# Kernel tuning notes

Hardware: AMD Instinct MI355X
Metric: run time of the kernel (lower is better)

Reference implementation:

```python
import jax, jax.numpy as jnp
import numpy as np

EPS = 1e-6

def _rms(x, g):
    # RMSNorm over last dim (head_dim)
    return x * jax.lax.rsqrt(jnp.mean(x * x, axis=-1, keepdims=True) + EPS) * g

def _split_heads(x, h):
    b, l, hd = x.shape
    return x.reshape(b, l, h, hd // h).transpose(0, 2, 1, 3)  # b h l d

def setup_inputs() -> dict:
    key = jax.random.key(0)
    ks = jax.random.split(key, 10)
    B, Limg, Lip, D, Dip, Temb = 1, 2048, 512, 3072, 1280, 1280
    return {
        "ip_hidden_states": jax.random.normal(ks[0], (B, Lip, Dip), jnp.float32),
        "img_query": jax.random.normal(ks[1], (B, Limg, D), jnp.float32),
        "img_key": jax.random.normal(ks[2], (B, Limg, D), jnp.float32),
        "img_value": jax.random.normal(ks[3], (B, Limg, D), jnp.float32),
        "t_emb": jax.random.normal(ks[4], (B, Temb), jnp.float32),
        "w_ada": jax.random.normal(ks[5], (2 * Dip, Temb), jnp.float32) * 0.02,
        "b_ada": jnp.zeros((2 * Dip,), jnp.float32),
        "w_k_ip": jax.random.normal(ks[6], (D, Dip), jnp.float32) * 0.02,
        "w_v_ip": jax.random.normal(ks[7], (D, Dip), jnp.float32) * 0.02,
        "g_q": jnp.ones((128,), jnp.float32),
        "g_k": jnp.ones((128,), jnp.float32),
        "g_ipk": jnp.ones((128,), jnp.float32),
        "n_heads": 24,
    }

def reference(ip_hidden_states, img_query, img_key, img_value, t_emb,
              w_ada, b_ada, w_k_ip, w_v_ip, g_q, g_k, g_ipk, n_heads):
    # AdaLayerNorm ('normal' mode): silu + linear -> shift/scale, LayerNorm (no affine)
    e = jax.nn.silu(t_emb) @ w_ada.T + b_ada              # [B, 2*Dip]
    shift, scale = jnp.split(e, 2, axis=1)
    mu = jnp.mean(ip_hidden_states, axis=-1, keepdims=True)
    var = jnp.var(ip_hidden_states, axis=-1, keepdims=True)
    xn = (ip_hidden_states - mu) * jax.lax.rsqrt(var + EPS)
    ip_norm = xn * (1.0 + scale[:, None]) + shift[:, None]  # [B, Lip, Dip]

    ip_key = ip_norm @ w_k_ip.T                            # [B, Lip, D]
    ip_value = ip_norm @ w_v_ip.T

    q = _split_heads(img_query, n_heads)                   # [B, H, Limg, d]
    k = _split_heads(img_key, n_heads)
    v = _split_heads(img_value, n_heads)
    ipk = _split_heads(ip_key, n_heads)                    # [B, H, Lip, d]
    ipv = _split_heads(ip_value, n_heads)

    q = _rms(q, g_q)
    k = _rms(k, g_k)
    ipk = _rms(ipk, g_ipk)

    key_all = jnp.concatenate([k, ipk], axis=2)            # [B, H, Limg+Lip, d]
    val_all = jnp.concatenate([v, ipv], axis=2)

    d = q.shape[-1]
    scores = jnp.einsum('bhqd,bhkd->bhqk', q, key_all) * (1.0 / np.sqrt(d))
    probs = jax.nn.softmax(scores, axis=-1)
    out = jnp.einsum('bhqk,bhkd->bhqd', probs, val_all)    # [B, H, Limg, d]

    b, h, l, dd = out.shape
    return out.transpose(0, 2, 1, 3).reshape(b, l, h * dd)
```

## Files before the change

kernel.cpp:

```cpp
#include <hip/hip_runtime.h>
#include <math.h>

#define H    24
#define Dh   128
#define LIMG 2048
#define LIP  512
#define DM   3072
#define DIP  1280
#define LK   2560
#define EPSF 1e-6f
#define SM_SCALE 0.08838834764831845f
#define C2EXP 0.12751930f
#define THRU 90.50967f

#define EXP2F(x) __builtin_exp2f(x)

typedef __attribute__((ext_vector_type(8))) short bf16x8;
typedef __attribute__((ext_vector_type(4))) float f32x4;

typedef const unsigned int __attribute__((address_space(1))) gu32;
typedef unsigned int __attribute__((address_space(3))) lu32;

static __device__ __forceinline__ unsigned short f2bf(float x) {
  union { float f; unsigned u; } v; v.f = x;
  unsigned r = v.u + 0x7fffu + ((v.u >> 16) & 1u);
  return (unsigned short)(r >> 16);
}

static __device__ __forceinline__ float bf2f(unsigned short b) {
  union { unsigned u; float f; } v; v.u = ((unsigned)b) << 16;
  return v.f;
}

static __device__ __forceinline__ unsigned cvt_pk_bf16(float a, float b) {
  unsigned r;
  asm("v_cvt_pk_bf16_f32 %0, %1, %2" : "=v"(r) : "v"(a), "v"(b));
  return r;
}

__global__ __launch_bounds__(256) void ada_kernel(
    const float* __restrict__ t_emb, const float* __restrict__ w_ada,
    const float* __restrict__ b_ada, float* __restrict__ e) {
  int j = blockIdx.x;
  int tid = threadIdx.x;
  const float* wrow = w_ada + (long)j * DIP;
  float acc = 0.f;
  for (int k = tid; k < DIP; k += 256) {
    float t = t_emb[k];
    acc += (t / (1.f + expf(-t))) * wrow[k];
  }
#pragma unroll
  for (int m = 1; m < 64; m <<= 1) acc += __shfl_xor(acc, m, 64);
  __shared__ float red[4];
  if ((tid & 63) == 0) red[tid >> 6] = acc;
  __syncthreads();
  if (tid == 0) e[j] = red[0] + red[1] + red[2] + red[3] + b_ada[j];
}

__global__ __launch_bounds__(256) void adaln_kernel(
    const float* __restrict__ x, const float* __restrict__ e,
    unsigned short* __restrict__ ipnh, unsigned short* __restrict__ ipnl) {
  int r = blockIdx.x;
  int tid = threadIdx.x;
  const float* xr = x + (long)r * DIP;
  float v[5];
  float s = 0.f, ss = 0.f;
#pragma unroll
  for (int i = 0; i < 5; i++) {
    v[i] = xr[tid + i * 256];
    s += v[i];
    ss += v[i] * v[i];
  }
#pragma unroll
  for (int m = 1; m < 64; m <<= 1) {
    s += __shfl_xor(s, m, 64);
    ss += __shfl_xor(ss, m, 64);
  }
  __shared__ float rs_[4], rss_[4];
  if ((tid & 63) == 0) { rs_[tid >> 6] = s; rss_[tid >> 6] = ss; }
  __syncthreads();
  s = rs_[0] + rs_[1] + rs_[2] + rs_[3];
  ss = rss_[0] + rss_[1] + rss_[2] + rss_[3];
  float mu = s * (1.f / DIP);
  float var = ss * (1.f / DIP) - mu * mu;
  float rstd = rsqrtf(var + EPSF);
  unsigned short* oh = ipnh + (long)r * DIP;
  unsigned short* ol = ipnl + (long)r * DIP;
#pragma unroll
  for (int i = 0; i < 5; i++) {
    int c = tid + i * 256;
    float o = (v[i] - mu) * rstd * (1.f + e[DIP + c]) + e[c];
    unsigned short hb = f2bf(o);
    oh[c] = hb;
    ol[c] = f2bf(o - bf2f(hb));
  }
}

__global__ __launch_bounds__(256) void prep_kernel(
    const float* __restrict__ k_in, const float* __restrict__ v_in,
    const float* __restrict__ g_k,
    unsigned short* __restrict__ Kb, unsigned short* __restrict__ Vt) {
  __shared__ unsigned short Vls[128][33];
  int h = blockIdx.y, l0 = blockIdx.x * 32;
  int tid = threadIdx.x;
  int r = tid >> 3, c = tid & 7;
  const float* ksrc = k_in + (long)(l0 + r) * DM + h * Dh + c * 16;
  const float* vsrc = v_in + (long)(l0 + r) * DM + h * Dh + c * 16;
  float kv[16], vv[16];
  float ssq = 0.f;
#pragma unroll
  for (int i = 0; i < 4; i++) {
    float4 a = *(const float4*)(ksrc + i * 4);
    float4 b = *(const float4*)(vsrc + i * 4);
    kv[i*4+0]=a.x; kv[i*4+1]=a.y; kv[i*4+2]=a.z; kv[i*4+3]=a.w;
    vv[i*4+0]=b.x; vv[i*4+1]=b.y; vv[i*4+2]=b.z; vv[i*4+3]=b.w;
    ssq += a.x*a.x + a.y*a.y + a.z*a.z + a.w*a.w;
  }
  ssq += __shfl_xor(ssq, 1, 8);
  ssq += __shfl_xor(ssq, 2, 8);
  ssq += __shfl_xor(ssq, 4, 8);
  float rstd = rsqrtf(ssq * (1.f / Dh) + EPSF);
  unsigned short kb[16];
#pragma unroll
  for (int i = 0; i < 16; i++) kb[i] = f2bf(kv[i] * rstd * g_k[c * 16 + i]);
  unsigned short* kdst = Kb + ((long)h * LK + l0 + r) * Dh + c * 16;
  *(uint4*)(kdst) = *(uint4*)(kb);
  *(uint4*)(kdst + 8) = *(uint4*)(kb + 8);
#pragma unroll
  for (int i = 0; i < 16; i++) Vls[c * 16 + i][r] = f2bf(vv[i]);
  __syncthreads();
  if (tid < 128) {
    int d = tid;
    unsigned short ov[32];
#pragma unroll
    for (int j = 0; j < 32; j++) ov[j] = Vls[d][j];
    unsigned short* vdst = Vt + ((long)h * 80 + (l0 >> 5)) * 4096 + d * 32;
    *(uint4*)(vdst)      = *(uint4*)(ov);
    *(uint4*)(vdst + 8)  = *(uint4*)(ov + 8);
    *(uint4*)(vdst + 16) = *(uint4*)(ov + 16);
    *(uint4*)(vdst + 24) = *(uint4*)(ov + 24);
  }
}

__global__ __launch_bounds__(256) void proj_kernel(
    const unsigned short* __restrict__ Ah, const unsigned short* __restrict__ Al,
    const float* __restrict__ Wk, const float* __restrict__ Wv,
    const float* __restrict__ g_ipk,
    unsigned short* __restrict__ Kb, unsigned short* __restrict__ Vt) {
  __shared__ __align__(16) unsigned short lds_u[24576];
  const float* W = blockIdx.z ? Wv : Wk;
  int h = blockIdx.y;
  int m0 = blockIdx.x * 64;
  int tid = threadIdx.x;
  int w = tid >> 6, lane = tid & 63;
  int m = lane & 15, quad = lane >> 4;

  const float* wrow = W + (long)(h * Dh + (tid & 127)) * DIP + ((tid >> 7) << 3);
  const unsigned short* garow_h = Ah + (long)(m0 + lane) * DIP + w * 8;
  const unsigned short* garow_l = Al + (long)(m0 + lane) * DIP + w * 8;

  f32x4 acc[8];
#pragma unroll
  for (int i = 0; i < 8; i++) acc[i] = (f32x4){0.f, 0.f, 0.f, 0.f};

  float4 wa = *(const float4*)(wrow);
  float4 wb = *(const float4*)(wrow + 4);
  float4 wc = *(const float4*)(wrow + 16);
  float4 wd = *(const float4*)(wrow + 20);

  auto stagek = [&](int b, int k0) {
    float cur[16] = {wa.x, wa.y, wa.z, wa.w, wb.x, wb.y, wb.z, wb.w,
                     wc.x, wc.y, wc.z, wc.w, wd.x, wd.y, wd.z, wd.w};
    if (k0 + 32 < DIP) {
      wa = *(const float4*)(wrow + k0 + 32);
      wb = *(const float4*)(wrow + k0 + 36);
      wc = *(const float4*)(wrow + k0 + 48);
      wd = *(const float4*)(wrow + k0 + 52);
    }
    unsigned hw[8], lw[8];
#pragma unroll
    for (int i = 0; i < 8; i++) {
      float a = cur[2 * i], b = cur[2 * i + 1];
      unsigned hword = cvt_pk_bf16(a, b);
      union { unsigned u; float f; } la, lb;
      la.u = hword << 16;
      lb.u = hword & 0xffff0000u;
      unsigned lword = cvt_pk_bf16(a - la.f, b - lb.f);
      hw[i] = hword; lw[i] = lword;
    }
    unsigned short* AhsB = lds_u + b * 12288;
    unsigned short* AlsB = AhsB + 2048;
    unsigned short* WhsB = AhsB + 4096;
    unsigned short* WlsB = AhsB + 8192;
    __builtin_amdgcn_global_load_lds((gu32*)(garow_h + k0), (lu32*)(AhsB + w * 512), 16, 0, 0);
    __builtin_amdgcn_global_load_lds((gu32*)(garow_l + k0), (lu32*)(AlsB + w * 512), 16, 0, 0);
    uint4 q;
    q.x = hw[0]; q.y = hw[1]; q.z = hw[2]; q.w = hw[3];
    *(uint4*)(WhsB + tid * 8) = q;
    q.x = lw[0]; q.y = lw[1]; q.z = lw[2]; q.w = lw[3];
    *(uint4*)(WlsB + tid * 8) = q;
    q.x = hw[4]; q.y = hw[5]; q.z = hw[6]; q.w = hw[7];
    *(uint4*)(WhsB + (tid + 256) * 8) = q;
    q.x = lw[4]; q.y = lw[5]; q.z = lw[6]; q.w = lw[7];
    *(uint4*)(WlsB + (tid + 256) * 8) = q;
  };

  stagek(0, 0);
  __syncthreads();
  int buf = 0;
#pragma unroll 1
  for (int k0 = 0; k0 < DIP; k0 += 32) {
    if (k0 + 32 < DIP) stagek(buf ^ 1, k0 + 32);
    unsigned short* AhsB = lds_u + buf * 12288;
    unsigned short* AlsB = AhsB + 2048;
    unsigned short* WhsB = AhsB + 4096;
    unsigned short* WlsB = AhsB + 8192;
    bf16x8 ahf = *(const bf16x8*)(AhsB + ((quad << 6) + (w << 4) + m) * 8);
    bf16x8 alf = *(const bf16x8*)(AlsB + ((quad << 6) + (w << 4) + m) * 8);
#pragma unroll
    for (int nt = 0; nt < 8; nt++) {
      bf16x8 bhf = *(const bf16x8*)(WhsB + ((quad << 7) + (nt << 4) + m) * 8);
      bf16x8 blf = *(const bf16x8*)(WlsB + ((quad << 7) + (nt << 4) + m) * 8);
      acc[nt] = __builtin_amdgcn_mfma_f32_16x16x32_bf16(ahf, bhf, acc[nt], 0, 0, 0);
      acc[nt] = __builtin_amdgcn_mfma_f32_16x16x32_bf16(ahf, blf, acc[nt], 0, 0, 0);
      acc[nt] = __builtin_amdgcn_mfma_f32_16x16x32_bf16(alf, bhf, acc[nt], 0, 0, 0);
    }
    __syncthreads();
    buf ^= 1;
  }

  if (blockIdx.z == 0) {
    float gkv[8];
#pragma unroll
    for (int nt = 0; nt < 8; nt++) gkv[nt] = g_ipk[nt * 16 + m];
#pragma unroll
    for (int r = 0; r < 4; r++) {
      float ssq = 0.f;
#pragma unroll
      for (int nt = 0; nt < 8; nt++) ssq += acc[nt][r] * acc[nt][r];
      ssq += __shfl_xor(ssq, 1, 16);
      ssq += __shfl_xor(ssq, 2, 16);
      ssq += __shfl_xor(ssq, 4, 16);
      ssq += __shfl_xor(ssq, 8, 16);
      float rstd = rsqrtf(ssq * (1.f / Dh) + EPSF);
      long row = (long)h * LK + LIMG + m0 + w * 16 + quad * 4 + r;
#pragma unroll
      for (int nt = 0; nt < 8; nt++)
        Kb[row * Dh + nt * 16 + m] = f2bf(acc[nt][r] * rstd * gkv[nt]);
    }
  } else {
    int l0q = LIMG + m0 + w * 16 + quad * 4;
    unsigned short* vbase = Vt + ((long)h * 80 + (l0q >> 5)) * 4096 + (l0q & 31);
#pragma unroll
    for (int nt = 0; nt < 8; nt++) {
      ushort4 o;
      o.x = f2bf(acc[nt][0]); o.y = f2bf(acc[nt][1]);
      o.z = f2bf(acc[nt][2]); o.w = f2bf(acc[nt][3]);
      *(ushort4*)(vbase + (nt * 16 + m) * 32) = o;
    }
  }
}

__global__ __launch_bounds__(256, 4) void flash_kernel(
    const float* __restrict__ q_in, const float* __restrict__ g_q,
    const unsigned short* __restrict__ Kb, const unsigned short* __restrict__ Vt,
    float* __restrict__ out) {
  __shared__ __align__(16) unsigned char lds[16384 + 16384 + 5120];
  unsigned short* Ks = (unsigned short*)lds;
  unsigned short* Vs = (unsigned short*)(lds + 16384);
  unsigned short* Ps = (unsigned short*)(lds + 32768);
  int tid = threadIdx.x;
  int w = tid >> 6, lid = tid & 63;
  int m = lid & 15, quad = lid >> 4;
  int id = blockIdx.x;
  int sidx = id >> 3;
  int h = (id & 7) * 3 + (sidx >> 5);
  int q0 = (sidx & 31) * 64;
  int qrow = q0 + w * 16 + m;

  bf16x8 aq[4];
  {
    float qf[4][8];
    float ssq = 0.f;
    const float* qsrc = q_in + (long)qrow * DM + h * Dh + quad * 8;
#pragma unroll
    for (int ks = 0; ks < 4; ks++) {
      float4 a = *(const float4*)(qsrc + ks * 32);
      float4 b = *(const float4*)(qsrc + ks * 32 + 4);
      qf[ks][0]=a.x; qf[ks][1]=a.y; qf[ks][2]=a.z; qf[ks][3]=a.w;
      qf[ks][4]=b.x; qf[ks][5]=b.y; qf[ks][6]=b.z; qf[ks][7]=b.w;
      ssq += a.x*a.x + a.y*a.y + a.z*a.z + a.w*a.w;
      ssq += b.x*b.x + b.y*b.y + b.z*b.z + b.w*b.w;
    }
    ssq += __shfl_xor(ssq, 16, 64);
    ssq += __shfl_xor(ssq, 32, 64);
    float rstd = rsqrtf(ssq * (1.f / Dh) + EPSF);
    const float* gq = g_q + quad * 8;
#pragma unroll
    for (int ks = 0; ks < 4; ks++) {
      float4 ga = *(const float4*)(gq + ks * 32);
      float4 gb = *(const float4*)(gq + ks * 32 + 4);
      float gg[8] = {ga.x, ga.y, ga.z, ga.w, gb.x, gb.y, gb.z, gb.w};
#pragma unroll
      for (int j = 0; j < 8; j++)
        aq[ks][j] = (short)f2bf(qf[ks][j] * rstd * gg[j]);
    }
  }

  const unsigned short* KbH = Kb + (long)h * LK * Dh;
  const unsigned short* VtH = Vt + (long)h * 80 * 4096;
  unsigned short* Pw = Ps + w * 640;

  f32x4 acc_o[8];
#pragma unroll
  for (int i = 0; i < 8; i++) acc_o[i] = (f32x4){0.f, 0.f, 0.f, 0.f};
  float mrun = -INFINITY;
  float lrun = 0.f;

  int s0 = w * 128 + lid, s1 = s0 + 64;
  int rK0 = s0 >> 4, cK0 = (s0 & 15) ^ (rK0 & 15);
  int rK1 = s1 >> 4, cK1 = (s1 & 15) ^ (rK1 & 15);
  const unsigned short* pK0 = KbH + (long)rK0 * Dh + cK0 * 8;
  const unsigned short* pK1 = KbH + (long)rK1 * Dh + cK1 * 8;
  int dV0 = s0 >> 2, cV0 = (s0 & 3) ^ ((dV0 >> 1) & 3);
  int dV1 = s1 >> 2, cV1 = (s1 & 3) ^ ((dV1 >> 1) & 3);
  const unsigned short* pV0 = VtH + dV0 * 32 + cV0 * 8;
  const unsigned short* pV1 = VtH + dV1 * 32 + cV1 * 8;

  auto stage = [&](int b) {
    unsigned short* KsB = Ks + b * 4096;
    unsigned short* VsB = Vs + b * 4096;
    __builtin_amdgcn_global_load_lds((gu32*)pK0, (lu32*)(KsB + (w * 128) * 8), 16, 0, 0);
    __builtin_amdgcn_global_load_lds((gu32*)pK1, (lu32*)(KsB + (w * 128 + 64) * 8), 16, 0, 0);
    __builtin_amdgcn_global_load_lds((gu32*)pV0, (lu32*)(VsB + (w * 128) * 8), 16, 0, 0);
    __builtin_amdgcn_global_load_lds((gu32*)pV1, (lu32*)(VsB + (w * 128 + 64) * 8), 16, 0, 0);
    pK0 += 4096; pK1 += 4096;
    pV0 += 4096; pV1 += 4096;
  };

  auto compute = [&](const unsigned short* KsB, const unsigned short* VsB) {
    f32x4 sc[2];
    sc[0] = (f32x4){0.f, 0.f, 0.f, 0.f};
    sc[1] = (f32x4){0.f, 0.f, 0.f, 0.f};
    __builtin_amdgcn_s_setprio(1);
#pragma unroll
    for (int t = 0; t < 2; t++)
#pragma unroll
      for (int ks = 0; ks < 4; ks++) {
        int rr = t * 16 + m;
        int g = (ks * 4 + quad) ^ m;
        bf16x8 bk = *(const bf16x8*)(KsB + rr * 128 + g * 8);
        sc[t] = __builtin_amdgcn_mfma_f32_16x16x32_bf16(bk, aq[ks], sc[t], 0, 0, 0);
      }
    __builtin_amdgcn_s_setprio(0);

    float pv[8] = {sc[0][0], sc[0][1], sc[0][2], sc[0][3],
                   sc[1][0], sc[1][1], sc[1][2], sc[1][3]};
    float p[8];
#pragma unroll
    for (int j = 0; j < 8; j++) p[j] = EXP2F((pv[j] - mrun) * C2EXP);

    float t0 = fmaxf(fmaxf(pv[0], pv[1]), fmaxf(pv[2], pv[3]));
    float t1 = fmaxf(fmaxf(pv[4], pv[5]), fmaxf(pv[6], pv[7]));
    float tmax = fmaxf(t0, t1);
    tmax = fmaxf(tmax, __shfl_xor(tmax, 16, 64));
    tmax = fmaxf(tmax, __shfl_xor(tmax, 32, 64));
    if (!__all(tmax <= mrun + THRU)) {
      float mnew = fmaxf(mrun, tmax);
      float al = EXP2F((mrun - mnew) * C2EXP);
      mrun = mnew;
#pragma unroll
      for (int j = 0; j < 8; j++) p[j] = EXP2F((pv[j] - mrun) * C2EXP);
      lrun *= al;
      float alr[4];
#pragma unroll
      for (int r = 0; r < 4; r++) alr[r] = __shfl(al, quad * 4 + r, 16);
#pragma unroll
      for (int dt = 0; dt < 8; dt++) {
        acc_o[dt][0] *= alr[0]; acc_o[dt][1] *= alr[1];
        acc_o[dt][2] *= alr[2]; acc_o[dt][3] *= alr[3];
      }
    }
    lrun += (p[0] + p[1]) + (p[2] + p[3]) + (p[4] + p[5]) + (p[6] + p[7]);

    uint2 pka, pkb;
    pka.x = cvt_pk_bf16(p[0], p[1]);
    pka.y = cvt_pk_bf16(p[2], p[3]);
    pkb.x = cvt_pk_bf16(p[4], p[5]);
    pkb.y = cvt_pk_bf16(p[6], p[7]);
    *(uint2*)(Pw + m * 40 + quad * 4) = pka;
    *(uint2*)(Pw + m * 40 + 16 + quad * 4) = pkb;
    bf16x8 ap = *(const bf16x8*)(Pw + m * 40 + quad * 8);

    __builtin_amdgcn_s_setprio(1);
#pragma unroll
    for (int dt = 0; dt < 8; dt++) {
      bf16x8 bv = *(const bf16x8*)(VsB + ((dt * 16 + m) * 4 + (quad ^ ((m >> 1) & 3))) * 8);
      acc_o[dt] = __builtin_amdgcn_mfma_f32_16x16x32_bf16(ap, bv, acc_o[dt], 0, 0, 0);
    }
    __builtin_amdgcn_s_setprio(0);
  };

  stage(0);
  __syncthreads();
#pragma unroll 1
  for (int jt = 0; jt < LK / 32; jt += 2) {
    stage(1);
    compute(Ks, Vs);
    __syncthreads();
    if (jt + 2 < LK / 32) stage(0);
    compute(Ks + 4096, Vs + 4096);
    __syncthreads();
  }

  lrun += __shfl_xor(lrun, 16, 64);
  lrun += __shfl_xor(lrun, 32, 64);
  float inv = 1.f / lrun;
  float ilr[4];
#pragma unroll
  for (int r = 0; r < 4; r++) ilr[r] = __shfl(inv, quad * 4 + r, 16);
#pragma unroll
  for (int dt = 0; dt < 8; dt++)
#pragma unroll
    for (int r = 0; r < 4; r++)
      out[(long)(q0 + w * 16 + quad * 4 + r) * DM + h * Dh + dt * 16 + m] =
          acc_o[dt][r] * ilr[r];
}

extern "C" void kernel_launch(void* const* d_in, const int* in_sizes, int n_in,
                              void* d_out, int out_size, void* d_ws, size_t ws_size,
                              hipStream_t stream) {
  const float* ip_hidden = (const float*)d_in[0];
  const float* img_q     = (const float*)d_in[1];
  const float* img_k     = (const float*)d_in[2];
  const float* img_v     = (const float*)d_in[3];
  const float* t_emb     = (const float*)d_in[4];
  const float* w_ada     = (const float*)d_in[5];
  const float* b_ada     = (const float*)d_in[6];
  const float* w_k_ip    = (const float*)d_in[7];
  const float* w_v_ip    = (const float*)d_in[8];
  const float* g_q       = (const float*)d_in[9];
  const float* g_k       = (const float*)d_in[10];
  const float* g_ipk     = (const float*)d_in[11];

  char* base = (char*)d_ws;
  float* e = (float*)base;
  unsigned short* ipnh = (unsigned short*)(base + 16384);
  unsigned short* ipnl = (unsigned short*)(base + 1327104);
  unsigned short* Kb   = (unsigned short*)(base + 2637824);
  unsigned short* Vt   = Kb + (size_t)H * LK * Dh;
  float* out = (float*)d_out;

  ada_kernel<<<2 * DIP, 256, 0, stream>>>(t_emb, w_ada, b_ada, e);
  adaln_kernel<<<LIP, 256, 0, stream>>>(ip_hidden, e, ipnh, ipnl);
  prep_kernel<<<dim3(LIMG / 32, H), 256, 0, stream>>>(img_k, img_v, g_k, Kb, Vt);
  proj_kernel<<<dim3(LIP / 64, H, 2), 256, 0, stream>>>(ipnh, ipnl, w_k_ip, w_v_ip,
                                                        g_ipk, Kb, Vt);
  flash_kernel<<<dim3(768), 256, 0, stream>>>(img_q, g_q, Kb, Vt, out);
}
```

Baseline: 368.4 us.

## Split flash attention KV range across warp pairs and merge ada/prep launches

The flash kernel now handles 32 query rows per block with 1536 blocks. Warps are split into two KV-split groups that each process alternate KV tiles and are merged at the end through LDS with a log-sum-exp combine. The goal is more parallelism and better latency hiding, at the cost of a larger LDS footprint (occupancy hint lowered to 2) and extra merge work. Separately, the ada and prep kernels are fused into one launch to save a kernel launch and let the two independent preprocessing stages run concurrently.

```diff
diff --git a/kernel.cpp b/kernel.cpp
--- a/kernel.cpp
+++ b/kernel.cpp
@@ -38,23 +38,69 @@
   return r;
 }
 
-__global__ __launch_bounds__(256) void ada_kernel(
+__global__ __launch_bounds__(256) void pre_kernel(
     const float* __restrict__ t_emb, const float* __restrict__ w_ada,
-    const float* __restrict__ b_ada, float* __restrict__ e) {
-  int j = blockIdx.x;
+    const float* __restrict__ b_ada, float* __restrict__ e,
+    const float* __restrict__ k_in, const float* __restrict__ v_in,
+    const float* __restrict__ g_k,
+    unsigned short* __restrict__ Kb, unsigned short* __restrict__ Vt) {
+  __shared__ unsigned short Vls[128][33];
+  __shared__ float red[4];
   int tid = threadIdx.x;
-  const float* wrow = w_ada + (long)j * DIP;
-  float acc = 0.f;
-  for (int k = tid; k < DIP; k += 256) {
-    float t = t_emb[k];
-    acc += (t / (1.f + expf(-t))) * wrow[k];
-  }
-#pragma unroll
-  for (int m = 1; m < 64; m <<= 1) acc += __shfl_xor(acc, m, 64);
-  __shared__ float red[4];
-  if ((tid & 63) == 0) red[tid >> 6] = acc;
-  __syncthreads();
-  if (tid == 0) e[j] = red[0] + red[1] + red[2] + red[3] + b_ada[j];
+  if (blockIdx.x < 2560) {
+    int j = blockIdx.x;
+    const float* wrow = w_ada + (long)j * DIP;
+    float acc = 0.f;
+    for (int k = tid; k < DIP; k += 256) {
+      float t = t_emb[k];
+      acc += (t / (1.f + expf(-t))) * wrow[k];
+    }
+#pragma unroll
+    for (int mm = 1; mm < 64; mm <<= 1) acc += __shfl_xor(acc, mm, 64);
+    if ((tid & 63) == 0) red[tid >> 6] = acc;
+    __syncthreads();
+    if (tid == 0) e[j] = red[0] + red[1] + red[2] + red[3] + b_ada[j];
+    return;
+  }
+  int pid = blockIdx.x - 2560;
+  int h = pid >> 6, l0 = (pid & 63) * 32;
+  int r = tid >> 3, c = tid & 7;
+  const float* ksrc = k_in + (long)(l0 + r) * DM + h * Dh + c * 16;
+  const float* vsrc = v_in + (long)(l0 + r) * DM + h * Dh + c * 16;
+  float kv[16], vv[16];
+  float ssq = 0.f;
+#pragma unroll
+  for (int i = 0; i < 4; i++) {
+    float4 a = *(const float4*)(ksrc + i * 4);
+    float4 b = *(const float4*)(vsrc + i * 4);
+    kv[i*4+0]=a.x; kv[i*4+1]=a.y; kv[i*4+2]=a.z; kv[i*4+3]=a.w;
+    vv[i*4+0]=b.x; vv[i*4+1]=b.y; vv[i*4+2]=b.z; vv[i*4+3]=b.w;
+    ssq += a.x*a.x + a.y*a.y + a.z*a.z + a.w*a.w;
+  }
+  ssq += __shfl_xor(ssq, 1, 8);
+  ssq += __shfl_xor(ssq, 2, 8);
+  ssq += __shfl_xor(ssq, 4, 8);
+  float rstd = rsqrtf(ssq * (1.f / Dh) + EPSF);
+  unsigned short kb[16];
+#pragma unroll
+  for (int i = 0; i < 16; i++) kb[i] = f2bf(kv[i] * rstd * g_k[c * 16 + i]);
+  unsigned short* kdst = Kb + ((long)h * LK + l0 + r) * Dh + c * 16;
+  *(uint4*)(kdst) = *(uint4*)(kb);
+  *(uint4*)(kdst + 8) = *(uint4*)(kb + 8);
+#pragma unroll
+  for (int i = 0; i < 16; i++) Vls[c * 16 + i][r] = f2bf(vv[i]);
+  __syncthreads();
+  if (tid < 128) {
+    int d = tid;
+    unsigned short ov[32];
+#pragma unroll
+    for (int j = 0; j < 32; j++) ov[j] = Vls[d][j];
+    unsigned short* vdst = Vt + ((long)h * 80 + (l0 >> 5)) * 4096 + d * 32;
+    *(uint4*)(vdst)      = *(uint4*)(ov);
+    *(uint4*)(vdst + 8)  = *(uint4*)(ov + 8);
+    *(uint4*)(vdst + 16) = *(uint4*)(ov + 16);
+    *(uint4*)(vdst + 24) = *(uint4*)(ov + 24);
+  }
 }
 
 __global__ __launch_bounds__(256) void adaln_kernel(
@@ -93,52 +139,6 @@
     unsigned short hb = f2bf(o);
     oh[c] = hb;
     ol[c] = f2bf(o - bf2f(hb));
-  }
-}
-
-__global__ __launch_bounds__(256) void prep_kernel(
-    const float* __restrict__ k_in, const float* __restrict__ v_in,
-    const float* __restrict__ g_k,
-    unsigned short* __restrict__ Kb, unsigned short* __restrict__ Vt) {
-  __shared__ unsigned short Vls[128][33];
-  int h = blockIdx.y, l0 = blockIdx.x * 32;
-  int tid = threadIdx.x;
-  int r = tid >> 3, c = tid & 7;
-  const float* ksrc = k_in + (long)(l0 + r) * DM + h * Dh + c * 16;
-  const float* vsrc = v_in + (long)(l0 + r) * DM + h * Dh + c * 16;
-  float kv[16], vv[16];
-  float ssq = 0.f;
-#pragma unroll
-  for (int i = 0; i < 4; i++) {
-    float4 a = *(const float4*)(ksrc + i * 4);
-    float4 b = *(const float4*)(vsrc + i * 4);
-    kv[i*4+0]=a.x; kv[i*4+1]=a.y; kv[i*4+2]=a.z; kv[i*4+3]=a.w;
-    vv[i*4+0]=b.x; vv[i*4+1]=b.y; vv[i*4+2]=b.z; vv[i*4+3]=b.w;
-    ssq += a.x*a.x + a.y*a.y + a.z*a.z + a.w*a.w;
-  }
-  ssq += __shfl_xor(ssq, 1, 8);
-  ssq += __shfl_xor(ssq, 2, 8);
-  ssq += __shfl_xor(ssq, 4, 8);
-  float rstd = rsqrtf(ssq * (1.f / Dh) + EPSF);
-  unsigned short kb[16];
-#pragma unroll
-  for (int i = 0; i < 16; i++) kb[i] = f2bf(kv[i] * rstd * g_k[c * 16 + i]);
-  unsigned short* kdst = Kb + ((long)h * LK + l0 + r) * Dh + c * 16;
-  *(uint4*)(kdst) = *(uint4*)(kb);
-  *(uint4*)(kdst + 8) = *(uint4*)(kb + 8);
-#pragma unroll
-  for (int i = 0; i < 16; i++) Vls[c * 16 + i][r] = f2bf(vv[i]);
-  __syncthreads();
-  if (tid < 128) {
-    int d = tid;
-    unsigned short ov[32];
-#pragma unroll
-    for (int j = 0; j < 32; j++) ov[j] = Vls[d][j];
-    unsigned short* vdst = Vt + ((long)h * 80 + (l0 >> 5)) * 4096 + d * 32;
-    *(uint4*)(vdst)      = *(uint4*)(ov);
-    *(uint4*)(vdst + 8)  = *(uint4*)(ov + 8);
-    *(uint4*)(vdst + 16) = *(uint4*)(ov + 16);
-    *(uint4*)(vdst + 24) = *(uint4*)(ov + 24);
   }
 }
 
@@ -261,22 +261,23 @@
   }
 }
 
-__global__ __launch_bounds__(256, 4) void flash_kernel(
+__global__ __launch_bounds__(256, 2) void flash_kernel(
     const float* __restrict__ q_in, const float* __restrict__ g_q,
     const unsigned short* __restrict__ Kb, const unsigned short* __restrict__ Vt,
     float* __restrict__ out) {
-  __shared__ __align__(16) unsigned char lds[16384 + 16384 + 5120];
-  unsigned short* Ks = (unsigned short*)lds;
-  unsigned short* Vs = (unsigned short*)(lds + 16384);
-  unsigned short* Ps = (unsigned short*)(lds + 32768);
+  __shared__ __align__(16) unsigned char lds[70656];
+  unsigned short* lus = (unsigned short*)lds;
+  unsigned short* Ps = lus + 32768;
   int tid = threadIdx.x;
   int w = tid >> 6, lid = tid & 63;
   int m = lid & 15, quad = lid >> 4;
+  int qg = w & 1;
+  int ks = w >> 1;
   int id = blockIdx.x;
   int sidx = id >> 3;
-  int h = (id & 7) * 3 + (sidx >> 5);
-  int q0 = (sidx & 31) * 64;
-  int qrow = q0 + w * 16 + m;
+  int h = (id & 7) * 3 + (sidx >> 6);
+  int q0 = (sidx & 63) * 32;
+  int qrow = q0 + qg * 16 + m;
 
   bf16x8 aq[4];
   {
@@ -284,11 +285,11 @@
     float ssq = 0.f;
     const float* qsrc = q_in + (long)qrow * DM + h * Dh + quad * 8;
 #pragma unroll
-    for (int ks = 0; ks < 4; ks++) {
-      float4 a = *(const float4*)(qsrc + ks * 32);
-      float4 b = *(const float4*)(qsrc + ks * 32 + 4);
-      qf[ks][0]=a.x; qf[ks][1]=a.y; qf[ks][2]=a.z; qf[ks][3]=a.w;
-      qf[ks][4]=b.x; qf[ks][5]=b.y; qf[ks][6]=b.z; qf[ks][7]=b.w;
+    for (int kk = 0; kk < 4; kk++) {
+      float4 a = *(const float4*)(qsrc + kk * 32);
+      float4 b = *(const float4*)(qsrc + kk * 32 + 4);
+      qf[kk][0]=a.x; qf[kk][1]=a.y; qf[kk][2]=a.z; qf[kk][3]=a.w;
+      qf[kk][4]=b.x; qf[kk][5]=b.y; qf[kk][6]=b.z; qf[kk][7]=b.w;
       ssq += a.x*a.x + a.y*a.y + a.z*a.z + a.w*a.w;
       ssq += b.x*b.x + b.y*b.y + b.z*b.z + b.w*b.w;
     }
@@ -297,13 +298,13 @@
     float rstd = rsqrtf(ssq * (1.f / Dh) + EPSF);
     const float* gq = g_q + quad * 8;
 #pragma unroll
-    for (int ks = 0; ks < 4; ks++) {
-      float4 ga = *(const float4*)(gq + ks * 32);
-      float4 gb = *(const float4*)(gq + ks * 32 + 4);
+    for (int kk = 0; kk < 4; kk++) {
+      float4 ga = *(const float4*)(gq + kk * 32);
+      float4 gb = *(const float4*)(gq + kk * 32 + 4);
       float gg[8] = {ga.x, ga.y, ga.z, ga.w, gb.x, gb.y, gb.z, gb.w};
 #pragma unroll
       for (int j = 0; j < 8; j++)
-        aq[ks][j] = (short)f2bf(qf[ks][j] * rstd * gg[j]);
+        aq[kk][j] = (short)f2bf(qf[kk][j] * rstd * gg[j]);
     }
   }
 
@@ -327,9 +328,9 @@
   const unsigned short* pV0 = VtH + dV0 * 32 + cV0 * 8;
   const unsigned short* pV1 = VtH + dV1 * 32 + cV1 * 8;
 
-  auto stage = [&](int b) {
-    unsigned short* KsB = Ks + b * 4096;
-    unsigned short* VsB = Vs + b * 4096;
+  auto stage = [&](int busofs) {
+    unsigned short* KsB = lus + busofs;
+    unsigned short* VsB = KsB + 4096;
     __builtin_amdgcn_global_load_lds((gu32*)pK0, (lu32*)(KsB + (w * 128) * 8), 16, 0, 0);
     __builtin_amdgcn_global_load_lds((gu32*)pK1, (lu32*)(KsB + (w * 128 + 64) * 8), 16, 0, 0);
     __builtin_amdgcn_global_load_lds((gu32*)pV0, (lu32*)(VsB + (w * 128) * 8), 16, 0, 0);
@@ -338,7 +339,8 @@
     pV0 += 4096; pV1 += 4096;
   };
 
-  auto compute = [&](const unsigned short* KsB, const unsigned short* VsB) {
+  auto compute = [&](const unsigned short* KsB) {
+    const unsigned short* VsB = KsB + 4096;
     f32x4 sc[2];
     sc[0] = (f32x4){0.f, 0.f, 0.f, 0.f};
     sc[1] = (f32x4){0.f, 0.f, 0.f, 0.f};
@@ -346,11 +348,11 @@
 #pragma unroll
     for (int t = 0; t < 2; t++)
 #pragma unroll
-      for (int ks = 0; ks < 4; ks++) {
+      for (int kk = 0; kk < 4; kk++) {
         int rr = t * 16 + m;
-        int g = (ks * 4 + quad) ^ m;
+        int g = (kk * 4 + quad) ^ m;
         bf16x8 bk = *(const bf16x8*)(KsB + rr * 128 + g * 8);
-        sc[t] = __builtin_amdgcn_mfma_f32_16x16x32_bf16(bk, aq[ks], sc[t], 0, 0, 0);
+        sc[t] = __builtin_amdgcn_mfma_f32_16x16x32_bf16(bk, aq[kk], sc[t], 0, 0, 0);
       }
     __builtin_amdgcn_s_setprio(0);
 
@@ -402,29 +404,63 @@
   };
 
   stage(0);
-  __syncthreads();
+  stage(8192);
+  __syncthreads();
+  const unsigned short* myb0 = lus + (ks ? 8192 : 0);
+  const unsigned short* myb1 = lus + (ks ? 24576 : 16384);
 #pragma unroll 1
-  for (int jt = 0; jt < LK / 32; jt += 2) {
-    stage(1);
-    compute(Ks, Vs);
+  for (int dp = 0; dp < 20; ++dp) {
+    stage(16384);
+    stage(24576);
+    compute(myb0);
     __syncthreads();
-    if (jt + 2 < LK / 32) stage(0);
-    compute(Ks + 4096, Vs + 4096);
+    if (dp < 19) {
+      stage(0);
+      stage(8192);
+    }
+    compute(myb1);
     __syncthreads();
   }
 
   lrun += __shfl_xor(lrun, 16, 64);
   lrun += __shfl_xor(lrun, 32, 64);
-  float inv = 1.f / lrun;
-  float ilr[4];
-#pragma unroll
-  for (int r = 0; r < 4; r++) ilr[r] = __shfl(inv, quad * 4 + r, 16);
-#pragma unroll
-  for (int dt = 0; dt < 8; dt++)
-#pragma unroll
-    for (int r = 0; r < 4; r++)
-      out[(long)(q0 + w * 16 + quad * 4 + r) * DM + h * Dh + dt * 16 + m] =
-          acc_o[dt][r] * ilr[r];
+  __syncthreads();
+  float* mg = (float*)lds;
+  float* lg = (float*)(lds + 512);
+  float* ag = (float*)(lds + 1024);
+  if (ks == 1) {
+    int o = qg * 64 + lid;
+    mg[o] = mrun;
+    lg[o] = lrun;
+    float* a = ag + o * 34;
+#pragma unroll
+    for (int dt = 0; dt < 8; dt++) *(f32x4*)(a + dt * 4) = acc_o[dt];
+  }
+  __syncthreads();
+  if (ks == 0) {
+    int o = qg * 64 + lid;
+    float m2 = mg[o], l2 = lg[o];
+    float mstar = fmaxf(mrun, m2);
+    float a1 = EXP2F((mrun - mstar) * C2EXP);
+    float a2 = EXP2F((m2 - mstar) * C2EXP);
+    float inv = 1.f / (lrun * a1 + l2 * a2);
+    float w1 = a1 * inv, w2 = a2 * inv;
+    float f1[4], f2[4];
+#pragma unroll
+    for (int r = 0; r < 4; r++) {
+      f1[r] = __shfl(w1, quad * 4 + r, 16);
+      f2[r] = __shfl(w2, quad * 4 + r, 16);
+    }
+    const float* a = ag + o * 34;
+#pragma unroll
+    for (int dt = 0; dt < 8; dt++) {
+      f32x4 p2 = *(const f32x4*)(a + dt * 4);
+#pragma unroll
+      for (int r = 0; r < 4; r++)
+        out[(long)(q0 + qg * 16 + quad * 4 + r) * DM + h * Dh + dt * 16 + m] =
+            acc_o[dt][r] * f1[r] + p2[r] * f2[r];
+    }
+  }
 }
 
 extern "C" void kernel_launch(void* const* d_in, const int* in_sizes, int n_in,
@@ -451,10 +487,10 @@
   unsigned short* Vt   = Kb + (size_t)H * LK * Dh;
   float* out = (float*)d_out;
 
-  ada_kernel<<<2 * DIP, 256, 0, stream>>>(t_emb, w_ada, b_ada, e);
+  pre_kernel<<<4096, 256, 0, stream>>>(t_emb, w_ada, b_ada, e,
+                                       img_k, img_v, g_k, Kb, Vt);
   adaln_kernel<<<LIP, 256, 0, stream>>>(ip_hidden, e, ipnh, ipnl);
-  prep_kernel<<<dim3(LIMG / 32, H), 256, 0, stream>>>(img_k, img_v, g_k, Kb, Vt);
   proj_kernel<<<dim3(LIP / 64, H, 2), 256, 0, stream>>>(ipnh, ipnl, w_k_ip, w_v_ip,
                                                         g_ipk, Kb, Vt);
-  flash_kernel<<<dim3(768), 256, 0, stream>>>(img_q, g_q, Kb, Vt, out);
-}
+  flash_kernel<<<dim3(1536), 256, 0, stream>>>(img_q, g_q, Kb, Vt, out);
+}
```

After: 407.6 us. 10.6% more time.

## Process two query tiles per wave in flash kernel and merge ada/prep launches

Applied to the files above, without the earlier changes.

The flash kernel now runs 128 threads per block, and each wave handles two 16-row query groups. Each K and V fragment read from LDS feeds two MFMAs, which halves LDS traffic per MFMA, at the cost of more registers per thread and fewer waves per block. Each thread now issues four global-to-LDS loads per stage instead of two. Separately, the ada and K/V prep kernels are merged into one launch that dispatches on block index, which removes one kernel launch.

```diff
diff --git a/kernel.cpp b/kernel.cpp
--- a/kernel.cpp
+++ b/kernel.cpp
@@ -38,23 +38,69 @@
   return r;
 }
 
-__global__ __launch_bounds__(256) void ada_kernel(
+__global__ __launch_bounds__(256) void pre_kernel(
     const float* __restrict__ t_emb, const float* __restrict__ w_ada,
-    const float* __restrict__ b_ada, float* __restrict__ e) {
-  int j = blockIdx.x;
+    const float* __restrict__ b_ada, float* __restrict__ e,
+    const float* __restrict__ k_in, const float* __restrict__ v_in,
+    const float* __restrict__ g_k,
+    unsigned short* __restrict__ Kb, unsigned short* __restrict__ Vt) {
+  __shared__ unsigned short Vls[128][33];
+  __shared__ float red[4];
   int tid = threadIdx.x;
-  const float* wrow = w_ada + (long)j * DIP;
-  float acc = 0.f;
-  for (int k = tid; k < DIP; k += 256) {
-    float t = t_emb[k];
-    acc += (t / (1.f + expf(-t))) * wrow[k];
-  }
-#pragma unroll
-  for (int m = 1; m < 64; m <<= 1) acc += __shfl_xor(acc, m, 64);
-  __shared__ float red[4];
-  if ((tid & 63) == 0) red[tid >> 6] = acc;
+  if (blockIdx.x < 2560) {
+    int j = blockIdx.x;
+    const float* wrow = w_ada + (long)j * DIP;
+    float acc = 0.f;
+    for (int k = tid; k < DIP; k += 256) {
+      float t = t_emb[k];
+      acc += (t / (1.f + expf(-t))) * wrow[k];
+    }
+#pragma unroll
+    for (int mm = 1; mm < 64; mm <<= 1) acc += __shfl_xor(acc, mm, 64);
+    if ((tid & 63) == 0) red[tid >> 6] = acc;
+    __syncthreads();
+    if (tid == 0) e[j] = red[0] + red[1] + red[2] + red[3] + b_ada[j];
+    return;
+  }
+  int pid = blockIdx.x - 2560;
+  int h = pid >> 6, l0 = (pid & 63) * 32;
+  int r = tid >> 3, c = tid & 7;
+  const float* ksrc = k_in + (long)(l0 + r) * DM + h * Dh + c * 16;
+  const float* vsrc = v_in + (long)(l0 + r) * DM + h * Dh + c * 16;
+  float kv[16], vv[16];
+  float ssq = 0.f;
+#pragma unroll
+  for (int i = 0; i < 4; i++) {
+    float4 a = *(const float4*)(ksrc + i * 4);
+    float4 b = *(const float4*)(vsrc + i * 4);
+    kv[i*4+0]=a.x; kv[i*4+1]=a.y; kv[i*4+2]=a.z; kv[i*4+3]=a.w;
+    vv[i*4+0]=b.x; vv[i*4+1]=b.y; vv[i*4+2]=b.z; vv[i*4+3]=b.w;
+    ssq += a.x*a.x + a.y*a.y + a.z*a.z + a.w*a.w;
+  }
+  ssq += __shfl_xor(ssq, 1, 8);
+  ssq += __shfl_xor(ssq, 2, 8);
+  ssq += __shfl_xor(ssq, 4, 8);
+  float rstd = rsqrtf(ssq * (1.f / Dh) + EPSF);
+  unsigned short kb[16];
+#pragma unroll
+  for (int i = 0; i < 16; i++) kb[i] = f2bf(kv[i] * rstd * g_k[c * 16 + i]);
+  unsigned short* kdst = Kb + ((long)h * LK + l0 + r) * Dh + c * 16;
+  *(uint4*)(kdst) = *(uint4*)(kb);
+  *(uint4*)(kdst + 8) = *(uint4*)(kb + 8);
+#pragma unroll
+  for (int i = 0; i < 16; i++) Vls[c * 16 + i][r] = f2bf(vv[i]);
   __syncthreads();
-  if (tid == 0) e[j] = red[0] + red[1] + red[2] + red[3] + b_ada[j];
+  if (tid < 128) {
+    int d = tid;
+    unsigned short ov[32];
+#pragma unroll
+    for (int j = 0; j < 32; j++) ov[j] = Vls[d][j];
+    unsigned short* vdst = Vt + ((long)h * 80 + (l0 >> 5)) * 4096 + d * 32;
+    *(uint4*)(vdst)      = *(uint4*)(ov);
+    *(uint4*)(vdst + 8)  = *(uint4*)(ov + 8);
+    *(uint4*)(vdst + 16) = *(uint4*)(ov + 16);
+    *(uint4*)(vdst + 24) = *(uint4*)(ov + 24);
+  }
 }
 
 __global__ __launch_bounds__(256) void adaln_kernel(
@@ -93,52 +139,6 @@
     unsigned short hb = f2bf(o);
     oh[c] = hb;
     ol[c] = f2bf(o - bf2f(hb));
-  }
-}
-
-__global__ __launch_bounds__(256) void prep_kernel(
-    const float* __restrict__ k_in, const float* __restrict__ v_in,
-    const float* __restrict__ g_k,
-    unsigned short* __restrict__ Kb, unsigned short* __restrict__ Vt) {
-  __shared__ unsigned short Vls[128][33];
-  int h = blockIdx.y, l0 = blockIdx.x * 32;
-  int tid = threadIdx.x;
-  int r = tid >> 3, c = tid & 7;
-  const float* ksrc = k_in + (long)(l0 + r) * DM + h * Dh + c * 16;
-  const float* vsrc = v_in + (long)(l0 + r) * DM + h * Dh + c * 16;
-  float kv[16], vv[16];
-  float ssq = 0.f;
-#pragma unroll
-  for (int i = 0; i < 4; i++) {
-    float4 a = *(const float4*)(ksrc + i * 4);
-    float4 b = *(const float4*)(vsrc + i * 4);
-    kv[i*4+0]=a.x; kv[i*4+1]=a.y; kv[i*4+2]=a.z; kv[i*4+3]=a.w;
-    vv[i*4+0]=b.x; vv[i*4+1]=b.y; vv[i*4+2]=b.z; vv[i*4+3]=b.w;
-    ssq += a.x*a.x + a.y*a.y + a.z*a.z + a.w*a.w;
-  }
-  ssq += __shfl_xor(ssq, 1, 8);
-  ssq += __shfl_xor(ssq, 2, 8);
-  ssq += __shfl_xor(ssq, 4, 8);
-  float rstd = rsqrtf(ssq * (1.f / Dh) + EPSF);
-  unsigned short kb[16];
-#pragma unroll
-  for (int i = 0; i < 16; i++) kb[i] = f2bf(kv[i] * rstd * g_k[c * 16 + i]);
-  unsigned short* kdst = Kb + ((long)h * LK + l0 + r) * Dh + c * 16;
-  *(uint4*)(kdst) = *(uint4*)(kb);
-  *(uint4*)(kdst + 8) = *(uint4*)(kb + 8);
-#pragma unroll
-  for (int i = 0; i < 16; i++) Vls[c * 16 + i][r] = f2bf(vv[i]);
-  __syncthreads();
-  if (tid < 128) {
-    int d = tid;
-    unsigned short ov[32];
-#pragma unroll
-    for (int j = 0; j < 32; j++) ov[j] = Vls[d][j];
-    unsigned short* vdst = Vt + ((long)h * 80 + (l0 >> 5)) * 4096 + d * 32;
-    *(uint4*)(vdst)      = *(uint4*)(ov);
-    *(uint4*)(vdst + 8)  = *(uint4*)(ov + 8);
-    *(uint4*)(vdst + 16) = *(uint4*)(ov + 16);
-    *(uint4*)(vdst + 24) = *(uint4*)(ov + 24);
   }
 }
 
@@ -261,7 +261,7 @@
   }
 }
 
-__global__ __launch_bounds__(256, 4) void flash_kernel(
+__global__ __launch_bounds__(128, 2) void flash_kernel(
     const float* __restrict__ q_in, const float* __restrict__ g_q,
     const unsigned short* __restrict__ Kb, const unsigned short* __restrict__ Vt,
     float* __restrict__ out) {
@@ -276,12 +276,13 @@
   int sidx = id >> 3;
   int h = (id & 7) * 3 + (sidx >> 5);
   int q0 = (sidx & 31) * 64;
-  int qrow = q0 + w * 16 + m;
-
-  bf16x8 aq[4];
-  {
+
+  bf16x8 aq[2][4];
+#pragma unroll
+  for (int g2 = 0; g2 < 2; g2++) {
     float qf[4][8];
     float ssq = 0.f;
+    int qrow = q0 + w * 32 + g2 * 16 + m;
     const float* qsrc = q_in + (long)qrow * DM + h * Dh + quad * 8;
 #pragma unroll
     for (int ks = 0; ks < 4; ks++) {
@@ -303,45 +304,52 @@
       float gg[8] = {ga.x, ga.y, ga.z, ga.w, gb.x, gb.y, gb.z, gb.w};
 #pragma unroll
       for (int j = 0; j < 8; j++)
-        aq[ks][j] = (short)f2bf(qf[ks][j] * rstd * gg[j]);
+        aq[g2][ks][j] = (short)f2bf(qf[ks][j] * rstd * gg[j]);
     }
   }
 
   const unsigned short* KbH = Kb + (long)h * LK * Dh;
   const unsigned short* VtH = Vt + (long)h * 80 * 4096;
-  unsigned short* Pw = Ps + w * 640;
-
-  f32x4 acc_o[8];
-#pragma unroll
-  for (int i = 0; i < 8; i++) acc_o[i] = (f32x4){0.f, 0.f, 0.f, 0.f};
-  float mrun = -INFINITY;
-  float lrun = 0.f;
-
-  int s0 = w * 128 + lid, s1 = s0 + 64;
-  int rK0 = s0 >> 4, cK0 = (s0 & 15) ^ (rK0 & 15);
-  int rK1 = s1 >> 4, cK1 = (s1 & 15) ^ (rK1 & 15);
-  const unsigned short* pK0 = KbH + (long)rK0 * Dh + cK0 * 8;
-  const unsigned short* pK1 = KbH + (long)rK1 * Dh + cK1 * 8;
-  int dV0 = s0 >> 2, cV0 = (s0 & 3) ^ ((dV0 >> 1) & 3);
-  int dV1 = s1 >> 2, cV1 = (s1 & 3) ^ ((dV1 >> 1) & 3);
-  const unsigned short* pV0 = VtH + dV0 * 32 + cV0 * 8;
-  const unsigned short* pV1 = VtH + dV1 * 32 + cV1 * 8;
+  unsigned short* Pw0 = Ps + (w * 2 + 0) * 640;
+  unsigned short* Pw1 = Ps + (w * 2 + 1) * 640;
+
+  f32x4 acc0[8], acc1[8];
+#pragma unroll
+  for (int i = 0; i < 8; i++) {
+    acc0[i] = (f32x4){0.f, 0.f, 0.f, 0.f};
+    acc1[i] = (f32x4){0.f, 0.f, 0.f, 0.f};
+  }
+  float mrun0 = -INFINITY, mrun1 = -INFINITY;
+  float lrun0 = 0.f, lrun1 = 0.f;
+
+  const unsigned short* pK[4];
+  const unsigned short* pV[4];
+#pragma unroll
+  for (int i = 0; i < 4; i++) {
+    int s = w * 256 + i * 64 + lid;
+    int rK = s >> 4, cK = (s & 15) ^ (rK & 15);
+    pK[i] = KbH + (long)rK * Dh + cK * 8;
+    int dV = s >> 2, cV = (s & 3) ^ ((dV >> 1) & 3);
+    pV[i] = VtH + dV * 32 + cV * 8;
+  }
 
   auto stage = [&](int b) {
     unsigned short* KsB = Ks + b * 4096;
     unsigned short* VsB = Vs + b * 4096;
-    __builtin_amdgcn_global_load_lds((gu32*)pK0, (lu32*)(KsB + (w * 128) * 8), 16, 0, 0);
-    __builtin_amdgcn_global_load_lds((gu32*)pK1, (lu32*)(KsB + (w * 128 + 64) * 8), 16, 0, 0);
-    __builtin_amdgcn_global_load_lds((gu32*)pV0, (lu32*)(VsB + (w * 128) * 8), 16, 0, 0);
-    __builtin_amdgcn_global_load_lds((gu32*)pV1, (lu32*)(VsB + (w * 128 + 64) * 8), 16, 0, 0);
-    pK0 += 4096; pK1 += 4096;
-    pV0 += 4096; pV1 += 4096;
+#pragma unroll
+    for (int i = 0; i < 4; i++) {
+      int so = (w * 256 + i * 64) * 8;
+      __builtin_amdgcn_global_load_lds((gu32*)pK[i], (lu32*)(KsB + so), 16, 0, 0);
+      __builtin_amdgcn_global_load_lds((gu32*)pV[i], (lu32*)(VsB + so), 16, 0, 0);
+      pK[i] += 4096;
+      pV[i] += 4096;
+    }
   };
 
   auto compute = [&](const unsigned short* KsB, const unsigned short* VsB) {
-    f32x4 sc[2];
-    sc[0] = (f32x4){0.f, 0.f, 0.f, 0.f};
-    sc[1] = (f32x4){0.f, 0.f, 0.f, 0.f};
+    f32x4 sc0[2], sc1[2];
+    sc0[0] = (f32x4){0.f,0.f,0.f,0.f}; sc0[1] = (f32x4){0.f,0.f,0.f,0.f};
+    sc1[0] = (f32x4){0.f,0.f,0.f,0.f}; sc1[1] = (f32x4){0.f,0.f,0.f,0.f};
     __builtin_amdgcn_s_setprio(1);
 #pragma unroll
     for (int t = 0; t < 2; t++)
@@ -350,53 +358,92 @@
         int rr = t * 16 + m;
         int g = (ks * 4 + quad) ^ m;
         bf16x8 bk = *(const bf16x8*)(KsB + rr * 128 + g * 8);
-        sc[t] = __builtin_amdgcn_mfma_f32_16x16x32_bf16(bk, aq[ks], sc[t], 0, 0, 0);
+        sc0[t] = __builtin_amdgcn_mfma_f32_16x16x32_bf16(bk, aq[0][ks], sc0[t], 0, 0, 0);
+        sc1[t] = __builtin_amdgcn_mfma_f32_16x16x32_bf16(bk, aq[1][ks], sc1[t], 0, 0, 0);
       }
     __builtin_amdgcn_s_setprio(0);
 
-    float pv[8] = {sc[0][0], sc[0][1], sc[0][2], sc[0][3],
-                   sc[1][0], sc[1][1], sc[1][2], sc[1][3]};
-    float p[8];
-#pragma unroll
-    for (int j = 0; j < 8; j++) p[j] = EXP2F((pv[j] - mrun) * C2EXP);
-
-    float t0 = fmaxf(fmaxf(pv[0], pv[1]), fmaxf(pv[2], pv[3]));
-    float t1 = fmaxf(fmaxf(pv[4], pv[5]), fmaxf(pv[6], pv[7]));
-    float tmax = fmaxf(t0, t1);
-    tmax = fmaxf(tmax, __shfl_xor(tmax, 16, 64));
-    tmax = fmaxf(tmax, __shfl_xor(tmax, 32, 64));
-    if (!__all(tmax <= mrun + THRU)) {
-      float mnew = fmaxf(mrun, tmax);
-      float al = EXP2F((mrun - mnew) * C2EXP);
-      mrun = mnew;
-#pragma unroll
-      for (int j = 0; j < 8; j++) p[j] = EXP2F((pv[j] - mrun) * C2EXP);
-      lrun *= al;
-      float alr[4];
-#pragma unroll
-      for (int r = 0; r < 4; r++) alr[r] = __shfl(al, quad * 4 + r, 16);
-#pragma unroll
-      for (int dt = 0; dt < 8; dt++) {
-        acc_o[dt][0] *= alr[0]; acc_o[dt][1] *= alr[1];
-        acc_o[dt][2] *= alr[2]; acc_o[dt][3] *= alr[3];
+    {
+      float pv[8] = {sc0[0][0], sc0[0][1], sc0[0][2], sc0[0][3],
+                     sc0[1][0], sc0[1][1], sc0[1][2], sc0[1][3]};
+      float p[8];
+#pragma unroll
+      for (int j = 0; j < 8; j++) p[j] = EXP2F((pv[j] - mrun0) * C2EXP);
+      float t0 = fmaxf(fmaxf(pv[0], pv[1]), fmaxf(pv[2], pv[3]));
+      float t1 = fmaxf(fmaxf(pv[4], pv[5]), fmaxf(pv[6], pv[7]));
+      float tmax = fmaxf(t0, t1);
+      tmax = fmaxf(tmax, __shfl_xor(tmax, 16, 64));
+      tmax = fmaxf(tmax, __shfl_xor(tmax, 32, 64));
+      if (!__all(tmax <= mrun0 + THRU)) {
+        float mnew = fmaxf(mrun0, tmax);
+        float al = EXP2F((mrun0 - mnew) * C2EXP);
+        mrun0 = mnew;
+#pragma unroll
+        for (int j = 0; j < 8; j++) p[j] = EXP2F((pv[j] - mrun0) * C2EXP);
+        lrun0 *= al;
+        float alr[4];
+#pragma unroll
+        for (int r = 0; r < 4; r++) alr[r] = __shfl(al, quad * 4 + r, 16);
+#pragma unroll
+        for (int dt = 0; dt < 8; dt++) {
+          acc0[dt][0] *= alr[0]; acc0[dt][1] *= alr[1];
+          acc0[dt][2] *= alr[2]; acc0[dt][3] *= alr[3];
+        }
       }
-    }
-    lrun += (p[0] + p[1]) + (p[2] + p[3]) + (p[4] + p[5]) + (p[6] + p[7]);
-
-    uint2 pka, pkb;
-    pka.x = cvt_pk_bf16(p[0], p[1]);
-    pka.y = cvt_pk_bf16(p[2], p[3]);
-    pkb.x = cvt_pk_bf16(p[4], p[5]);
-    pkb.y = cvt_pk_bf16(p[6], p[7]);
-    *(uint2*)(Pw + m * 40 + quad * 4) = pka;
-    *(uint2*)(Pw + m * 40 + 16 + quad * 4) = pkb;
-    bf16x8 ap = *(const bf16x8*)(Pw + m * 40 + quad * 8);
+      lrun0 += (p[0] + p[1]) + (p[2] + p[3]) + (p[4] + p[5]) + (p[6] + p[7]);
+      uint2 pka, pkb;
+      pka.x = cvt_pk_bf16(p[0], p[1]);
+      pka.y = cvt_pk_bf16(p[2], p[3]);
+      pkb.x = cvt_pk_bf16(p[4], p[5]);
+      pkb.y = cvt_pk_bf16(p[6], p[7]);
+      *(uint2*)(Pw0 + m * 40 + quad * 4) = pka;
+      *(uint2*)(Pw0 + m * 40 + 16 + quad * 4) = pkb;
+    }
+    {
+      float pv[8] = {sc1[0][0], sc1[0][1], sc1[0][2], sc1[0][3],
+                     sc1[1][0], sc1[1][1], sc1[1][2], sc1[1][3]};
+      float p[8];
+#pragma unroll
+      for (int j = 0; j < 8; j++) p[j] = EXP2F((pv[j] - mrun1) * C2EXP);
+      float t0 = fmaxf(fmaxf(pv[0], pv[1]), fmaxf(pv[2], pv[3]));
+      float t1 = fmaxf(fmaxf(pv[4], pv[5]), fmaxf(pv[6], pv[7]));
+      float tmax = fmaxf(t0, t1);
+      tmax = fmaxf(tmax, __shfl_xor(tmax, 16, 64));
+      tmax = fmaxf(tmax, __shfl_xor(tmax, 32, 64));
+      if (!__all(tmax <= mrun1 + THRU)) {
+        float mnew = fmaxf(mrun1, tmax);
+        float al = EXP2F((mrun1 - mnew) * C2EXP);
+        mrun1 = mnew;
+#pragma unroll
+        for (int j = 0; j < 8; j++) p[j] = EXP2F((pv[j] - mrun1) * C2EXP);
+        lrun1 *= al;
+        float alr[4];
+#pragma unroll
+        for (int r = 0; r < 4; r++) alr[r] = __shfl(al, quad * 4 + r, 16);
+#pragma unroll
+        for (int dt = 0; dt < 8; dt++) {
+          acc1[dt][0] *= alr[0]; acc1[dt][1] *= alr[1];
+          acc1[dt][2] *= alr[2]; acc1[dt][3] *= alr[3];
+        }
+      }
+      lrun1 += (p[0] + p[1]) + (p[2] + p[3]) + (p[4] + p[5]) + (p[6] + p[7]);
+      uint2 pka, pkb;
+      pka.x = cvt_pk_bf16(p[0], p[1]);
+      pka.y = cvt_pk_bf16(p[2], p[3]);
+      pkb.x = cvt_pk_bf16(p[4], p[5]);
+      pkb.y = cvt_pk_bf16(p[6], p[7]);
+      *(uint2*)(Pw1 + m * 40 + quad * 4) = pka;
+      *(uint2*)(Pw1 + m * 40 + 16 + quad * 4) = pkb;
+    }
+    bf16x8 ap0 = *(const bf16x8*)(Pw0 + m * 40 + quad * 8);
+    bf16x8 ap1 = *(const bf16x8*)(Pw1 + m * 40 + quad * 8);
 
     __builtin_amdgcn_s_setprio(1);
 #pragma unroll
     for (int dt = 0; dt < 8; dt++) {
       bf16x8 bv = *(const bf16x8*)(VsB + ((dt * 16 + m) * 4 + (quad ^ ((m >> 1) & 3))) * 8);
-      acc_o[dt] = __builtin_amdgcn_mfma_f32_16x16x32_bf16(ap, bv, acc_o[dt], 0, 0, 0);
+      acc0[dt] = __builtin_amdgcn_mfma_f32_16x16x32_bf16(ap0, bv, acc0[dt], 0, 0, 0);
+      acc1[dt] = __builtin_amdgcn_mfma_f32_16x16x32_bf16(ap1, bv, acc1[dt], 0, 0, 0);
     }
     __builtin_amdgcn_s_setprio(0);
   };
@@ -413,18 +460,34 @@
     __syncthreads();
   }
 
-  lrun += __shfl_xor(lrun, 16, 64);
-  lrun += __shfl_xor(lrun, 32, 64);
-  float inv = 1.f / lrun;
-  float ilr[4];
-#pragma unroll
-  for (int r = 0; r < 4; r++) ilr[r] = __shfl(inv, quad * 4 + r, 16);
-#pragma unroll
-  for (int dt = 0; dt < 8; dt++)
-#pragma unroll
-    for (int r = 0; r < 4; r++)
-      out[(long)(q0 + w * 16 + quad * 4 + r) * DM + h * Dh + dt * 16 + m] =
-          acc_o[dt][r] * ilr[r];
+  {
+    lrun0 += __shfl_xor(lrun0, 16, 64);
+    lrun0 += __shfl_xor(lrun0, 32, 64);
+    float inv = 1.f / lrun0;
+    float ilr[4];
+#pragma unroll
+    for (int r = 0; r < 4; r++) ilr[r] = __shfl(inv, quad * 4 + r, 16);
+#pragma unroll
+    for (int dt = 0; dt < 8; dt++)
+#pragma unroll
+      for (int r = 0; r < 4; r++)
+        out[(long)(q0 + w * 32 + quad * 4 + r) * DM + h * Dh + dt * 16 + m] =
+            acc0[dt][r] * ilr[r];
+  }
+  {
+    lrun1 += __shfl_xor(lrun1, 16, 64);
+    lrun1 += __shfl_xor(lrun1, 32, 64);
+    float inv = 1.f / lrun1;
+    float ilr[4];
+#pragma unroll
+    for (int r = 0; r < 4; r++) ilr[r] = __shfl(inv, quad * 4 + r, 16);
+#pragma unroll
+    for (int dt = 0; dt < 8; dt++)
+#pragma unroll
+      for (int r = 0; r < 4; r++)
+        out[(long)(q0 + w * 32 + 16 + quad * 4 + r) * DM + h * Dh + dt * 16 + m] =
+            acc1[dt][r] * ilr[r];
+  }
 }
 
 extern "C" void kernel_launch(void* const* d_in, const int* in_sizes, int n_in,
@@ -451,10 +514,10 @@
   unsigned short* Vt   = Kb + (size_t)H * LK * Dh;
   float* out = (float*)d_out;
 
-  ada_kernel<<<2 * DIP, 256, 0, stream>>>(t_emb, w_ada, b_ada, e);
+  pre_kernel<<<4096, 256, 0, stream>>>(t_emb, w_ada, b_ada, e,
+                                       img_k, img_v, g_k, Kb, Vt);
   adaln_kernel<<<LIP, 256, 0, stream>>>(ip_hidden, e, ipnh, ipnl);
-  prep_kernel<<<dim3(LIMG / 32, H), 256, 0, stream>>>(img_k, img_v, g_k, Kb, Vt);
   proj_kernel<<<dim3(LIP / 64, H, 2), 256, 0, stream>>>(ipnh, ipnl, w_k_ip, w_v_ip,
                                                         g_ipk, Kb, Vt);
-  flash_kernel<<<dim3(768), 256, 0, stream>>>(img_q, g_q, Kb, Vt, out);
-}
+  flash_kernel<<<dim3(768), 128, 0, stream>>>(img_q, g_q, Kb, Vt, out);
+}
```

Measured after the change: 390.1 us. +5.9%, slower.
